# Performance work log

Measured on AMD Instinct MI355X. Metric: run time of the kernel, lower is better.

The kernel has to match this reference:

```python
import jax, jax.numpy as jnp
import numpy as np

B, T, D_MODEL = 2, 2048, 2048
N_HEADS, N_KV, HEAD_DIM = 16, 8, 128
ROPE_BASE = 10000.0
LAMBDA_INIT = 0.2  # 0.8 - 0.6*exp(-0.3*0), layer_depth=0


def rms_norm(x):
    eps = jnp.finfo(x.dtype).eps
    return x * jax.lax.rsqrt(jnp.mean(x * x, axis=-1, keepdims=True) + eps)


def rope_cos_sin(seq_len, dim):
    inv_freq = 1.0 / (ROPE_BASE ** (np.arange(0, dim, 2, dtype=np.float32) / dim))
    t = np.arange(seq_len, dtype=np.float32)
    freqs = np.outer(t, inv_freq)  # [T, dim/2]
    # original caches cos/sin in bfloat16
    cos = jnp.asarray(np.cos(freqs)).astype(jnp.bfloat16).astype(jnp.float32)
    sin = jnp.asarray(np.sin(freqs)).astype(jnp.bfloat16).astype(jnp.float32)
    return cos[None, :, None, :], sin[None, :, None, :]


def apply_rotary(x, cos, sin):
    d = x.shape[-1] // 2
    x1, x2 = x[..., :d], x[..., d:]
    return jnp.concatenate([x1 * cos + x2 * sin, -x1 * sin + x2 * cos], axis=-1)


def causal_attn(q, k, v):
    # q: [B,T,H,Dq], k: [B,S,H,Dq], v: [B,S,H,Dv]
    scale = 1.0 / np.sqrt(q.shape[-1]).astype(np.float32)
    s = jnp.einsum('bthd,bshd->bhts', q, k) * scale
    mask = jnp.tril(jnp.ones((q.shape[1], k.shape[1]), dtype=bool))
    s = jnp.where(mask, s, -jnp.inf)
    p = jax.nn.softmax(s, axis=-1)
    return jnp.einsum('bhts,bshe->bthe', p, v)


def diff_attention(x, Wq, Wk, Wv, lambda_q1, lambda_k1, lambda_q2, lambda_k2, softmax_scaler):
    b, t, _ = x.shape
    q = (x @ Wq.T).reshape(b, t, N_HEADS, HEAD_DIM)
    k = (x @ Wk.T).reshape(b, t, N_KV, HEAD_DIM)
    v = (x @ Wv.T).reshape(b, t, N_KV // 2, 2 * HEAD_DIM)
    cos, sin = rope_cos_sin(t, HEAD_DIM)
    q, k = rms_norm(q), rms_norm(k)
    q, k = apply_rotary(q, cos, sin), apply_rotary(k, cos, sin)
    k = k.reshape(b, t, 2, N_KV // 2, HEAD_DIM)
    k1, k2 = k[:, :, 0], k[:, :, 1]
    # scalable softmax: q *= scaler_h * log(position)
    pos = jnp.arange(1, t + 1, dtype=jnp.float32).reshape(1, t, 1, 1)
    q = softmax_scaler.reshape(1, 1, -1, 1) * jnp.log(pos) * q
    q = q.reshape(b, t, 2, N_HEADS // 2, HEAD_DIM)
    q1, q2 = q[:, :, 0], q[:, :, 1]
    rep = N_HEADS // N_KV  # GQA repeat
    k1 = jnp.repeat(k1, rep, axis=2)
    k2 = jnp.repeat(k2, rep, axis=2)
    vr = jnp.repeat(v, rep, axis=2)
    y1 = causal_attn(q1, k1, vr)
    y2 = causal_attn(q2, k2, vr)
    lam1 = jnp.exp(jnp.sum(lambda_q1 * lambda_k1))
    lam2 = jnp.exp(jnp.sum(lambda_q2 * lambda_k2))
    lam = lam1 - lam2 + LAMBDA_INIT
    return y1 - lam * y2  # [B,T,N_HEADS//2, 2*HEAD_DIM]


def setup_inputs() -> dict:
    key = jax.random.key(0)
    ks = jax.random.split(key, 8)
    return {
        'x': jax.random.normal(ks[0], (B, T, D_MODEL), dtype=jnp.float32),
        'Wq': jax.random.normal(ks[1], (N_HEADS * HEAD_DIM, D_MODEL), dtype=jnp.float32) * 0.02,
        'Wk': jax.random.normal(ks[2], (N_KV * HEAD_DIM, D_MODEL), dtype=jnp.float32) * 0.02,
        'Wv': jax.random.normal(ks[3], (N_KV * HEAD_DIM, D_MODEL), dtype=jnp.float32) * 0.02,
        'lambda_q1': jax.random.normal(ks[4], (HEAD_DIM // 2,), dtype=jnp.float32) * 0.1,
        'lambda_k1': jax.random.normal(ks[5], (HEAD_DIM // 2,), dtype=jnp.float32) * 0.1,
        'lambda_q2': jax.random.normal(ks[6], (HEAD_DIM // 2,), dtype=jnp.float32) * 0.1,
        'lambda_k2': jax.random.normal(ks[7], (HEAD_DIM // 2,), dtype=jnp.float32) * 0.1,
        'softmax_scaler': jnp.ones((N_HEADS,), dtype=jnp.float32),
    }


def reference(x, Wq, Wk, Wv, lambda_q1, lambda_k1, lambda_q2, lambda_k2, softmax_scaler):
    return diff_attention(x, Wq, Wk, Wv, lambda_q1, lambda_k1, lambda_q2, lambda_k2, softmax_scaler)
```

## Files before the change

kernel.cpp:

```cpp
#include <hip/hip_runtime.h>

#define T_SEQ 2048
#define DMODEL 2048
#define BSZ 2
#define MROWS (BSZ * T_SEQ)
#define NQKV 4096
#define NEG_BIG (-1e30f)

typedef __attribute__((ext_vector_type(8))) _Float16 half8;
typedef __attribute__((ext_vector_type(4))) _Float16 half4;
typedef __attribute__((ext_vector_type(4))) float f32x4;

typedef const __attribute__((address_space(1))) unsigned int* gas_ptr;
typedef __attribute__((address_space(3))) unsigned int* las_ptr;
#define GLD16(g, l) __builtin_amdgcn_global_load_lds((gas_ptr)(g), (las_ptr)(l), 16, 0, 0)

__device__ __forceinline__ unsigned short f2bf(float f) {
  unsigned u = __float_as_uint(f);
  unsigned r = (u + 0x7fffu + ((u >> 16) & 1u)) >> 16;
  return (unsigned short)r;
}
__device__ __forceinline__ float bf2f(unsigned short h) {
  return __uint_as_float(((unsigned)h) << 16);
}

__global__ void build_rope(float* __restrict__ cosT, float* __restrict__ sinT) {
  int t = blockIdx.x;
  int i = threadIdx.x;
  float inv = (float)pow(10000.0, -((double)(2 * i)) / 128.0);
  float fr = (float)t * inv;
  cosT[t * 64 + i] = bf2f(f2bf(cosf(fr)));
  sinT[t * 64 + i] = bf2f(f2bf(sinf(fr)));
}

__global__ __launch_bounds__(256) void cvt_xw(const float* __restrict__ x,
                                              const float* __restrict__ Wq,
                                              const float* __restrict__ Wk,
                                              const float* __restrict__ Wv,
                                              _Float16* __restrict__ xh,
                                              _Float16* __restrict__ wh) {
  int bid = blockIdx.x;
  size_t o = ((size_t)(bid & 4095) * 256 + threadIdx.x) * 8;
  const float* src;
  _Float16* dst;
  if (bid < 4096) {
    src = x + o;
    dst = xh + o;
  } else {
    int row = (int)(o >> 11), col = (int)(o & 2047);
    src = ((row < 2048) ? (Wq + (size_t)row * 2048)
          : (row < 3072) ? (Wk + (size_t)(row - 2048) * 2048)
                         : (Wv + (size_t)(row - 3072) * 2048)) + col;
    dst = wh + o;
  }
  float4 v0 = *(const float4*)(src);
  float4 v1 = *(const float4*)(src + 4);
  half8 r;
  r[0] = (_Float16)v0.x; r[1] = (_Float16)v0.y; r[2] = (_Float16)v0.z; r[3] = (_Float16)v0.w;
  r[4] = (_Float16)v1.x; r[5] = (_Float16)v1.y; r[6] = (_Float16)v1.z; r[7] = (_Float16)v1.w;
  *(half8*)(dst) = r;
}

__global__ __launch_bounds__(256) void gemm_nt(const _Float16* __restrict__ A,
                                               const _Float16* __restrict__ Bw,
                                               _Float16* __restrict__ C) {
  const int K = DMODEL, N = NQKV;
  __shared__ __align__(16) char As[2][128 * 128];
  __shared__ __align__(16) char Bs[2][128 * 128];
  int tid = threadIdx.x;
  int lane = tid & 63, w = tid >> 6;
  int wm = w >> 1, wn = w & 1;
  int l15 = lane & 15, quad = lane >> 4;
  int bm = blockIdx.y, bn = blockIdx.x;

  const char* Aab = (const char*)(A + (size_t)(bm * 128) * K);
  const char* Bab = (const char*)(Bw + (size_t)(bn * 128) * K);
  int srow = lane >> 3;
  int scol = ((lane & 7) ^ srow) << 4;

  auto stage = [&](int t) {
    int buf = t & 1;
    size_t kb = (size_t)t << 7;
#pragma unroll
    for (int g = 0; g < 4; g++) {
      int row = w * 32 + g * 8 + srow;
      GLD16(Aab + (size_t)row * (K * 2) + kb + scol, &As[buf][w * 4096 + g * 1024]);
    }
#pragma unroll
    for (int g = 0; g < 4; g++) {
      int row = w * 32 + g * 8 + srow;
      GLD16(Bab + (size_t)row * (K * 2) + kb + scol, &Bs[buf][w * 4096 + g * 1024]);
    }
  };

  f32x4 acc[4][4];
#pragma unroll
  for (int i = 0; i < 4; i++)
#pragma unroll
    for (int j = 0; j < 4; j++) acc[i][j] = (f32x4){0.f, 0.f, 0.f, 0.f};

  stage(0);
  for (int t = 0; t < 32; t++) {
    if (t < 31) {
      stage(t + 1);
      asm volatile("s_waitcnt vmcnt(8)" ::: "memory");
    } else {
      asm volatile("s_waitcnt vmcnt(0)" ::: "memory");
    }
    __builtin_amdgcn_s_barrier();
    __builtin_amdgcn_sched_barrier(0);

    const char* ab = As[t & 1];
    const char* bb = Bs[t & 1];
#pragma unroll
    for (int kc = 0; kc < 2; kc++) {
      half8 af[4], bfr[4];
#pragma unroll
      for (int i = 0; i < 4; i++) {
        int row = wm * 64 + i * 16 + l15;
        af[i] = *(const half8*)(ab + row * 128 + ((kc * 64 + quad * 16) ^ ((row & 7) << 4)));
      }
#pragma unroll
      for (int j = 0; j < 4; j++) {
        int row = wn * 64 + j * 16 + l15;
        bfr[j] = *(const half8*)(bb + row * 128 + ((kc * 64 + quad * 16) ^ ((row & 7) << 4)));
      }
#pragma unroll
      for (int i = 0; i < 4; i++)
#pragma unroll
        for (int j = 0; j < 4; j++)
          acc[i][j] = __builtin_amdgcn_mfma_f32_16x16x32_f16(af[i], bfr[j], acc[i][j], 0, 0, 0);
    }

    asm volatile("s_waitcnt lgkmcnt(0)" ::: "memory");
    __builtin_amdgcn_s_barrier();
    __builtin_amdgcn_sched_barrier(0);
  }

#pragma unroll
  for (int i = 0; i < 4; i++)
#pragma unroll
    for (int j = 0; j < 4; j++)
#pragma unroll
      for (int r = 0; r < 4; r++) {
        int row = bm * 128 + wm * 64 + i * 16 + quad * 4 + r;
        int col = bn * 128 + wn * 64 + j * 16 + l15;
        C[(size_t)row * N + col] = (_Float16)acc[i][j][r];
      }
}

__global__ __launch_bounds__(128) void postproc(_Float16* __restrict__ qkv,
                                                const float* __restrict__ cosT,
                                                const float* __restrict__ sinT,
                                                _Float16* __restrict__ kp) {
  int t = blockIdx.x, h = blockIdx.y, b = blockIdx.z;
  int d = threadIdx.x;
  int col = (h < 16) ? (h * 128 + d) : (2048 + (h - 16) * 128 + d);
  size_t idx = ((size_t)(b * T_SEQ + t)) * NQKV + col;
  float v = (float)qkv[idx];
  float ss = v * v;
#pragma unroll
  for (int m = 1; m < 64; m <<= 1) ss += __shfl_xor(ss, m, 64);
  __shared__ float sred[2];
  __shared__ float xs[128];
  if ((threadIdx.x & 63) == 0) sred[threadIdx.x >> 6] = ss;
  __syncthreads();
  float total = sred[0] + sred[1];
  float rn = rsqrtf(total * (1.0f / 128.0f) + 1.1920929e-7f);
  float xn = v * rn;
  xs[d] = xn;
  __syncthreads();
  float o;
  if (d < 64) {
    float c = cosT[t * 64 + d], s = sinT[t * 64 + d];
    o = xn * c + xs[d + 64] * s;
  } else {
    float c = cosT[t * 64 + d - 64], s = sinT[t * 64 + d - 64];
    o = -xs[d - 64] * s + xn * c;
  }
  if (h < 16)
    qkv[idx] = (_Float16)o;
  else
    kp[(((size_t)(b * 8 + (h - 16))) * T_SEQ + t) * 128 + d] = (_Float16)o;
}

__global__ void transpose_v(const _Float16* __restrict__ qkv,
                            _Float16* __restrict__ vt) {
  __shared__ _Float16 tile[32][33];
  int t0 = blockIdx.x * 32, d0 = blockIdx.y * 32;
  int bz = blockIdx.z;
  int b = bz >> 2, vh = bz & 3;
  int tx = threadIdx.x, ty = threadIdx.y;
#pragma unroll
  for (int i = 0; i < 4; i++) {
    int t = t0 + ty + i * 8;
    tile[ty + i * 8][tx] = qkv[((size_t)(b * T_SEQ + t)) * NQKV + 3072 + vh * 256 + d0 + tx];
  }
  __syncthreads();
#pragma unroll
  for (int i = 0; i < 4; i++) {
    int d = d0 + ty + i * 8;
    vt[(((size_t)(b * 4 + vh)) * 256 + d) * T_SEQ + t0 + tx] = tile[tx][ty + i * 8];
  }
}

__global__ __launch_bounds__(256) void attn(const _Float16* __restrict__ qkv,
                                            const _Float16* __restrict__ kp,
                                            const _Float16* __restrict__ vt,
                                            const float* __restrict__ scaler,
                                            float* __restrict__ y1out,
                                            _Float16* __restrict__ y2out) {
  __shared__ __align__(16) char Ks[2][64 * 256];
  __shared__ __align__(16) char Vs[2][128 * 128];
  __shared__ _Float16 Pt[4 * 16 * 72];

  int tid = threadIdx.x, lane = tid & 63, w = tid >> 6;
  int l15 = lane & 15, quad = lane >> 4;
  int bx = blockIdx.x, hh = blockIdx.y, z = blockIdx.z;
  int b = z >> 1, br = z & 1;
  int qh = br * 8 + hh;
  int kh = br * 4 + (hh >> 1);
  int vh = hh >> 1;

  const char* kbase_b = (const char*)(kp + ((size_t)(b * 8 + kh)) * T_SEQ * 128);
  const char* vbase_b = (const char*)(vt + ((size_t)(b * 4 + vh)) * 256 * T_SEQ);
  _Float16* pw = &Pt[w * 16 * 72];
  float sc = scaler[qh] * 0.08838834764831844f;

  int krow_l = lane >> 4;
  int kpc    = (lane & 15) << 4;
  int vrow_l = lane >> 3;
  int vpc    = (lane & 7) << 4;

  auto stageK = [&](int kt1) {
    int ksr = kt1 * 64;
    char* dstb = Ks[kt1 & 1];
#pragma unroll
    for (int c2 = 0; c2 < 4; c2++) {
      int c = w * 4 + c2;
      int row = c * 4 + krow_l;
      const char* src = kbase_b + (((size_t)(ksr + row)) << 8) + (kpc ^ ((row & 7) << 4));
      GLD16(src, dstb + (c << 10));
    }
  };
  auto stageV = [&](int kt1) {
    int ksb = kt1 * 128;
#pragma unroll
    for (int h = 0; h < 2; h++)
#pragma unroll
      for (int c2 = 0; c2 < 4; c2++) {
        int c = w * 4 + c2;
        int d = h * 128 + c * 8 + vrow_l;
        const char* src = vbase_b + (size_t)d * (T_SEQ * 2) + ksb + (vpc ^ (vrow_l << 4));
        GLD16(src, Vs[h] + (c << 10));
      }
  };

  for (int half = 0; half < 2; half++) {
    int qt = half ? (31 - bx) : bx;
    int t0 = qt * 64;
    int tg = t0 + w * 16 + l15;

    const _Float16* qbase = qkv + ((size_t)(b * T_SEQ + tg)) * NQKV + qh * 128;
    half8 qf[4];
#pragma unroll
    for (int kc = 0; kc < 4; kc++)
      qf[kc] = *(const half8*)(qbase + kc * 32 + quad * 8);

    stageK(0);
    stageV(0);
    __builtin_amdgcn_sched_barrier(0);

    float mrow = NEG_BIG, lrow = 0.f;
    float rowscale = sc * logf((float)(tg + 1));
    f32x4 acc[16];
#pragma unroll
    for (int nb = 0; nb < 16; nb++) acc[nb] = (f32x4){0.f, 0.f, 0.f, 0.f};

    for (int kt = 0; kt <= qt; kt++) {
      int ks = kt * 64;
      bool notlast = (kt < qt);

      asm volatile("s_waitcnt vmcnt(8)" ::: "memory");
      __builtin_amdgcn_s_barrier();
      __builtin_amdgcn_sched_barrier(0);
      if (notlast) stageK(kt + 1);

      const char* kbuf = Ks[kt & 1];
      f32x4 sv[4];
#pragma unroll
      for (int j = 0; j < 4; j++) {
        int row = j * 16 + l15;
        int sw = (row & 7) << 4;
        const char* kr = kbuf + (row << 8);
        half8 kf0 = *(const half8*)(kr + (((quad << 4) + 0) ^ sw));
        half8 kf1 = *(const half8*)(kr + (((quad << 4) + 64) ^ sw));
        half8 kf2 = *(const half8*)(kr + (((quad << 4) + 128) ^ sw));
        half8 kf3 = *(const half8*)(kr + (((quad << 4) + 192) ^ sw));
        f32x4 a = (f32x4){0.f, 0.f, 0.f, 0.f};
        a = __builtin_amdgcn_mfma_f32_16x16x32_f16(kf0, qf[0], a, 0, 0, 0);
        a = __builtin_amdgcn_mfma_f32_16x16x32_f16(kf1, qf[1], a, 0, 0, 0);
        a = __builtin_amdgcn_mfma_f32_16x16x32_f16(kf2, qf[2], a, 0, 0, 0);
        a = __builtin_amdgcn_mfma_f32_16x16x32_f16(kf3, qf[3], a, 0, 0, 0);
        sv[j] = a;
      }

      bool diag = (kt == qt);
      float s_r[16];
      float mx = NEG_BIG;
#pragma unroll
      for (int j = 0; j < 4; j++)
#pragma unroll
        for (int r = 0; r < 4; r++) {
          float s = sv[j][r] * rowscale;
          if (diag) {
            int kg = ks + j * 16 + quad * 4 + r;
            if (kg > tg) s = NEG_BIG;
          }
          s_r[j * 4 + r] = s;
          mx = fmaxf(mx, s);
        }
      mx = fmaxf(mx, __shfl_xor(mx, 16, 64));
      mx = fmaxf(mx, __shfl_xor(mx, 32, 64));
      float mnew = fmaxf(mrow, mx);
      float alpha = __expf(mrow - mnew);
      float p[16];
      float rs = 0.f;
#pragma unroll
      for (int i = 0; i < 16; i++) {
        p[i] = __expf(s_r[i] - mnew);
        rs += p[i];
      }
      rs += __shfl_xor(rs, 16, 64);
      rs += __shfl_xor(rs, 32, 64);
      lrow = lrow * alpha + rs;
      mrow = mnew;
      float at[4];
#pragma unroll
      for (int r = 0; r < 4; r++) at[r] = __shfl(alpha, quad * 20 + r, 64);
#pragma unroll
      for (int nb = 0; nb < 16; nb++)
#pragma unroll
        for (int r = 0; r < 4; r++) acc[nb][r] *= at[r];

#pragma unroll
      for (int j = 0; j < 4; j++) {
        half4 pk;
        pk[0] = (_Float16)p[j * 4 + 0];
        pk[1] = (_Float16)p[j * 4 + 1];
        pk[2] = (_Float16)p[j * 4 + 2];
        pk[3] = (_Float16)p[j * 4 + 3];
        *(half4*)&pw[l15 * 72 + j * 16 + quad * 4] = pk;
      }
      half8 pf0 = *(const half8*)&pw[l15 * 72 + quad * 8];
      half8 pf1 = *(const half8*)&pw[l15 * 72 + 32 + quad * 8];

      if (notlast)
        asm volatile("s_waitcnt vmcnt(4)" ::: "memory");
      else
        asm volatile("s_waitcnt vmcnt(0)" ::: "memory");
      __builtin_amdgcn_s_barrier();
      __builtin_amdgcn_sched_barrier(0);

#pragma unroll
      for (int h = 0; h < 2; h++) {
#pragma unroll
        for (int nbl = 0; nbl < 8; nbl++) {
          int row = nbl * 16 + l15;
          int sw = (row & 7) << 4;
          const char* vr = Vs[h] + (row << 7);
          half8 vf0 = *(const half8*)(vr + (((quad << 4) + 0) ^ sw));
          half8 vf1 = *(const half8*)(vr + (((quad << 4) + 64) ^ sw));
          int nb = h * 8 + nbl;
          acc[nb] = __builtin_amdgcn_mfma_f32_16x16x32_f16(pf0, vf0, acc[nb], 0, 0, 0);
          acc[nb] = __builtin_amdgcn_mfma_f32_16x16x32_f16(pf1, vf1, acc[nb], 0, 0, 0);
        }
      }

      asm volatile("s_waitcnt lgkmcnt(0)" ::: "memory");
      __builtin_amdgcn_s_barrier();
      __builtin_amdgcn_sched_barrier(0);
      if (notlast) stageV(kt + 1);
    }

    float linv = 1.0f / lrow;
    float lt[4];
#pragma unroll
    for (int r = 0; r < 4; r++) lt[r] = __shfl(linv, quad * 20 + r, 64);
#pragma unroll
    for (int r = 0; r < 4; r++) {
      int tr = t0 + w * 16 + quad * 4 + r;
      size_t base = ((size_t)(b * T_SEQ + tr)) * 2048 + hh * 256;
      if (br) {
#pragma unroll
        for (int nb = 0; nb < 16; nb++)
          y2out[base + nb * 16 + l15] = (_Float16)(acc[nb][r] * lt[r]);
      } else {
#pragma unroll
        for (int nb = 0; nb < 16; nb++)
          y1out[base + nb * 16 + l15] = acc[nb][r] * lt[r];
      }
    }
  }
}

__global__ __launch_bounds__(256) void combine(float* __restrict__ out,
                                               const _Float16* __restrict__ y2,
                                               const float* __restrict__ lq1,
                                               const float* __restrict__ lk1,
                                               const float* __restrict__ lq2,
                                               const float* __restrict__ lk2) {
  int lane = threadIdx.x & 63;
  float a = lq1[lane] * lk1[lane];
  float bb = lq2[lane] * lk2[lane];
#pragma unroll
  for (int m = 1; m < 64; m <<= 1) {
    a += __shfl_xor(a, m, 64);
    bb += __shfl_xor(bb, m, 64);
  }
  float lam = expf(a) - expf(bb) + 0.2f;

  size_t o = ((size_t)blockIdx.x * 256 + threadIdx.x) * 8;
  half8 yv = *(const half8*)(y2 + o);
  float4 a0 = *(float4*)(out + o);
  float4 a1 = *(float4*)(out + o + 4);
  a0.x -= lam * (float)yv[0];
  a0.y -= lam * (float)yv[1];
  a0.z -= lam * (float)yv[2];
  a0.w -= lam * (float)yv[3];
  a1.x -= lam * (float)yv[4];
  a1.y -= lam * (float)yv[5];
  a1.z -= lam * (float)yv[6];
  a1.w -= lam * (float)yv[7];
  *(float4*)(out + o) = a0;
  *(float4*)(out + o + 4) = a1;
}

extern "C" void kernel_launch(void* const* d_in, const int* in_sizes, int n_in,
                              void* d_out, int out_size, void* d_ws, size_t ws_size,
                              hipStream_t stream) {
  const float* x   = (const float*)d_in[0];
  const float* Wq  = (const float*)d_in[1];
  const float* Wk  = (const float*)d_in[2];
  const float* Wv  = (const float*)d_in[3];
  const float* lq1 = (const float*)d_in[4];
  const float* lk1 = (const float*)d_in[5];
  const float* lq2 = (const float*)d_in[6];
  const float* lk2 = (const float*)d_in[7];
  const float* scaler = (const float*)d_in[8];
  float* out = (float*)d_out;

  char* W = (char*)d_ws;
  _Float16* xh   = (_Float16*)(W + 0);
  _Float16* wh   = (_Float16*)(W + 16777216);
  _Float16* qkvh = (_Float16*)(W + 33554432);
  _Float16* kph  = (_Float16*)(W + 0);
  _Float16* vtb  = (_Float16*)(W + 8388608);
  _Float16* y2h  = (_Float16*)(W + 16777216);
  float* cosT    = out;
  float* sinT    = out + 131072;

  build_rope<<<T_SEQ, 64, 0, stream>>>(cosT, sinT);
  cvt_xw<<<8192, 256, 0, stream>>>(x, Wq, Wk, Wv, xh, wh);
  gemm_nt<<<dim3(NQKV / 128, MROWS / 128), 256, 0, stream>>>(xh, wh, qkvh);
  postproc<<<dim3(T_SEQ, 24, BSZ), 128, 0, stream>>>(qkvh, cosT, sinT, kph);
  transpose_v<<<dim3(T_SEQ / 32, 256 / 32, BSZ * 4), dim3(32, 8), 0, stream>>>(qkvh, vtb);
  attn<<<dim3(16, 8, BSZ * 2), 256, 0, stream>>>(qkvh, kph, vtb, scaler, out, y2h);
  combine<<<4096, 256, 0, stream>>>(out, y2h, lq1, lk1, lq2, lk2);
}
```

Measured before the change: 330.1 us.

## Vectorize RMSNorm/RoPE postproc, remap attention grid, use exp2 with lazy rescale

Postproc now handles 16 tokens per 256-thread block, using half8 vector loads and stores and a lane shuffle for the RoPE partner instead of LDS plus two barriers. The attention launch becomes a 1D grid that is remapped to (q-tile, head, batch/branch) to change block scheduling order and cache locality. Softmax folds log2(e) into the row scale and uses exp2f. Accumulator rescaling is skipped unless the running max grows by more than 8, which trades extra VALU work for a bounded risk of fp16 P overflow (values up to 2^8).

```diff
diff --git a/kernel.cpp b/kernel.cpp
--- a/kernel.cpp
+++ b/kernel.cpp
@@ -149,39 +149,48 @@
       }
 }
 
-__global__ __launch_bounds__(128) void postproc(_Float16* __restrict__ qkv,
+__global__ __launch_bounds__(256) void postproc(_Float16* __restrict__ qkv,
                                                 const float* __restrict__ cosT,
                                                 const float* __restrict__ sinT,
                                                 _Float16* __restrict__ kp) {
-  int t = blockIdx.x, h = blockIdx.y, b = blockIdx.z;
-  int d = threadIdx.x;
-  int col = (h < 16) ? (h * 128 + d) : (2048 + (h - 16) * 128 + d);
-  size_t idx = ((size_t)(b * T_SEQ + t)) * NQKV + col;
-  float v = (float)qkv[idx];
-  float ss = v * v;
-#pragma unroll
-  for (int m = 1; m < 64; m <<= 1) ss += __shfl_xor(ss, m, 64);
-  __shared__ float sred[2];
-  __shared__ float xs[128];
-  if ((threadIdx.x & 63) == 0) sred[threadIdx.x >> 6] = ss;
-  __syncthreads();
-  float total = sred[0] + sred[1];
-  float rn = rsqrtf(total * (1.0f / 128.0f) + 1.1920929e-7f);
-  float xn = v * rn;
-  xs[d] = xn;
-  __syncthreads();
-  float o;
-  if (d < 64) {
-    float c = cosT[t * 64 + d], s = sinT[t * 64 + d];
-    o = xn * c + xs[d + 64] * s;
-  } else {
-    float c = cosT[t * 64 + d - 64], s = sinT[t * 64 + d - 64];
-    o = -xs[d - 64] * s + xn * c;
+  int tid = threadIdx.x, lane = tid & 63, w = tid >> 6;
+  int h = blockIdx.y;
+  int tkn = blockIdx.x * 16 + w * 4 + (lane >> 4);
+  int b = tkn >> 11, t = tkn & 2047;
+  int l15 = lane & 15;
+  int col0 = (h < 16) ? (h * 128) : (2048 + (h - 16) * 128);
+  size_t base = (size_t)tkn * NQKV + col0 + l15 * 8;
+
+  half8 v = *(const half8*)(qkv + base);
+  float xf[8];
+  float ss = 0.f;
+#pragma unroll
+  for (int j = 0; j < 8; j++) { xf[j] = (float)v[j]; ss += xf[j] * xf[j]; }
+  ss += __shfl_xor(ss, 1, 64);
+  ss += __shfl_xor(ss, 2, 64);
+  ss += __shfl_xor(ss, 4, 64);
+  ss += __shfl_xor(ss, 8, 64);
+  float rn = rsqrtf(ss * (1.0f / 128.0f) + 1.1920929e-7f);
+
+  const float* cb = cosT + t * 64 + (lane & 7) * 8;
+  const float* sb = sinT + t * 64 + (lane & 7) * 8;
+  float4 c0 = *(const float4*)cb, c1 = *(const float4*)(cb + 4);
+  float4 s0 = *(const float4*)sb, s1 = *(const float4*)(sb + 4);
+  float cc[8] = {c0.x, c0.y, c0.z, c0.w, c1.x, c1.y, c1.z, c1.w};
+  float sn[8] = {s0.x, s0.y, s0.z, s0.w, s1.x, s1.y, s1.z, s1.w};
+  float sgn = (lane & 8) ? -1.f : 1.f;
+
+  half8 o;
+#pragma unroll
+  for (int j = 0; j < 8; j++) {
+    float xn = xf[j] * rn;
+    float xp = __shfl_xor(xn, 8, 64);
+    o[j] = (_Float16)(xn * cc[j] + sgn * xp * sn[j]);
   }
   if (h < 16)
-    qkv[idx] = (_Float16)o;
+    *(half8*)(qkv + base) = o;
   else
-    kp[(((size_t)(b * 8 + (h - 16))) * T_SEQ + t) * 128 + d] = (_Float16)o;
+    *(half8*)(kp + (((size_t)(b * 8 + (h - 16))) * T_SEQ + t) * 128 + l15 * 8) = o;
 }
 
 __global__ void transpose_v(const _Float16* __restrict__ qkv,
@@ -216,7 +225,10 @@
 
   int tid = threadIdx.x, lane = tid & 63, w = tid >> 6;
   int l15 = lane & 15, quad = lane >> 4;
-  int bx = blockIdx.x, hh = blockIdx.y, z = blockIdx.z;
+  int lin = blockIdx.x;
+  int c = (lin & 7) * 4 + ((lin >> 3) & 3);
+  int bx = lin >> 5;
+  int hh = c & 7, z = c >> 3;
   int b = z >> 1, br = z & 1;
   int qh = br * 8 + hh;
   int kh = br * 4 + (hh >> 1);
@@ -237,10 +249,10 @@
     char* dstb = Ks[kt1 & 1];
 #pragma unroll
     for (int c2 = 0; c2 < 4; c2++) {
-      int c = w * 4 + c2;
-      int row = c * 4 + krow_l;
+      int cc = w * 4 + c2;
+      int row = cc * 4 + krow_l;
       const char* src = kbase_b + (((size_t)(ksr + row)) << 8) + (kpc ^ ((row & 7) << 4));
-      GLD16(src, dstb + (c << 10));
+      GLD16(src, dstb + (cc << 10));
     }
   };
   auto stageV = [&](int kt1) {
@@ -249,10 +261,10 @@
     for (int h = 0; h < 2; h++)
 #pragma unroll
       for (int c2 = 0; c2 < 4; c2++) {
-        int c = w * 4 + c2;
-        int d = h * 128 + c * 8 + vrow_l;
+        int cc = w * 4 + c2;
+        int d = h * 128 + cc * 8 + vrow_l;
         const char* src = vbase_b + (size_t)d * (T_SEQ * 2) + ksb + (vpc ^ (vrow_l << 4));
-        GLD16(src, Vs[h] + (c << 10));
+        GLD16(src, Vs[h] + (cc << 10));
       }
   };
 
@@ -272,7 +284,7 @@
     __builtin_amdgcn_sched_barrier(0);
 
     float mrow = NEG_BIG, lrow = 0.f;
-    float rowscale = sc * logf((float)(tg + 1));
+    float rowscale = sc * logf((float)(tg + 1)) * 1.44269504f;
     f32x4 acc[16];
 #pragma unroll
     for (int nb = 0; nb < 16; nb++) acc[nb] = (f32x4){0.f, 0.f, 0.f, 0.f};
@@ -322,26 +334,29 @@
         }
       mx = fmaxf(mx, __shfl_xor(mx, 16, 64));
       mx = fmaxf(mx, __shfl_xor(mx, 32, 64));
-      float mnew = fmaxf(mrow, mx);
-      float alpha = __expf(mrow - mnew);
+      if (__any(mx > mrow + 8.0f)) {
+        float mnew = fmaxf(mrow, mx);
+        float alpha = exp2f(mrow - mnew);
+        mrow = mnew;
+        lrow *= alpha;
+        float at[4];
+#pragma unroll
+        for (int r = 0; r < 4; r++) at[r] = __shfl(alpha, quad * 20 + r, 64);
+#pragma unroll
+        for (int nb = 0; nb < 16; nb++)
+#pragma unroll
+          for (int r = 0; r < 4; r++) acc[nb][r] *= at[r];
+      }
       float p[16];
       float rs = 0.f;
 #pragma unroll
       for (int i = 0; i < 16; i++) {
-        p[i] = __expf(s_r[i] - mnew);
+        p[i] = exp2f(s_r[i] - mrow);
         rs += p[i];
       }
       rs += __shfl_xor(rs, 16, 64);
       rs += __shfl_xor(rs, 32, 64);
-      lrow = lrow * alpha + rs;
-      mrow = mnew;
-      float at[4];
-#pragma unroll
-      for (int r = 0; r < 4; r++) at[r] = __shfl(alpha, quad * 20 + r, 64);
-#pragma unroll
-      for (int nb = 0; nb < 16; nb++)
-#pragma unroll
-        for (int r = 0; r < 4; r++) acc[nb][r] *= at[r];
+      lrow += rs;
 
 #pragma unroll
       for (int j = 0; j < 4; j++) {
@@ -463,8 +478,8 @@
   build_rope<<<T_SEQ, 64, 0, stream>>>(cosT, sinT);
   cvt_xw<<<8192, 256, 0, stream>>>(x, Wq, Wk, Wv, xh, wh);
   gemm_nt<<<dim3(NQKV / 128, MROWS / 128), 256, 0, stream>>>(xh, wh, qkvh);
-  postproc<<<dim3(T_SEQ, 24, BSZ), 128, 0, stream>>>(qkvh, cosT, sinT, kph);
+  postproc<<<dim3(256, 24), 256, 0, stream>>>(qkvh, cosT, sinT, kph);
   transpose_v<<<dim3(T_SEQ / 32, 256 / 32, BSZ * 4), dim3(32, 8), 0, stream>>>(qkvh, vtb);
-  attn<<<dim3(16, 8, BSZ * 2), 256, 0, stream>>>(qkvh, kph, vtb, scaler, out, y2h);
+  attn<<<512, 256, 0, stream>>>(qkvh, kph, vtb, scaler, out, y2h);
   combine<<<4096, 256, 0, stream>>>(out, y2h, lq1, lk1, lq2, lk2);
 }
```

Measured after the change: 367.2 us. 11.2% more time.
